# Kernel tuning notes

Hardware: AMD Instinct MI355X
Metric: run time of the kernel (lower is better)

## Reference

```python
import jax, jax.numpy as jnp
import numpy as np

RANK = 8
NUM_MORPH = 10000   # morpheme vocab (num_embeddings)
CORE_DIM = 8        # ceil(512 ** (1/3))
ORDER = 3
NUM_SURF = 50000    # word vocab (num_surfaces)
EMB_DIM = 512
LN_EPS = 1e-5
BATCH, SEQ = 8, 2048


def setup_inputs() -> dict:
    key = jax.random.key(0)
    kx, kc, kw = jax.random.split(key, 3)
    # token ids over the word vocabulary
    x = jax.random.randint(kx, (BATCH, SEQ), 0, NUM_SURF, dtype=jnp.int64)
    # word -> morpheme-id mapping, one id per tensor-train order position
    co_matrix = jax.random.randint(kc, (NUM_SURF, ORDER), 0, NUM_MORPH, dtype=jnp.int64)
    # xavier_uniform over (rank, num_morph, core_dim): fan_in = num_morph*core_dim, fan_out = rank*core_dim
    bound = float(np.sqrt(6.0 / (NUM_MORPH * CORE_DIM + RANK * CORE_DIM)))
    weight = jax.random.uniform(kw, (RANK, NUM_MORPH, CORE_DIM), dtype=jnp.float32,
                                minval=-bound, maxval=bound)
    weight = weight.at[:, 0].set(0.0)  # reset_parameters zeroes morpheme index 0
    ln_scale = jnp.ones((EMB_DIM,), dtype=jnp.float32)
    ln_bias = jnp.zeros((EMB_DIM,), dtype=jnp.float32)
    return {"x": x, "co_matrix": co_matrix, "weight": weight,
            "ln_scale": ln_scale, "ln_bias": ln_bias}


def _emb_matrix(weight, co_matrix, ln_scale, ln_bias):
    # gather all order cores at once: [rank, num_surf, order, core_dim]
    cores = weight[:, co_matrix, :]
    w = cores[:, :, 0, :]                                  # [R, S, C]
    for i in range(1, ORDER):
        # order-wise broadcast outer product, flattened feature dim grows C^i
        w = (w[:, :, :, None] * cores[:, :, i, None, :]).reshape(RANK, NUM_SURF, -1)
    w = w.sum(axis=0)[:, :EMB_DIM]                         # [S, EMB_DIM]
    mu = jnp.mean(w, axis=-1, keepdims=True)
    var = jnp.var(w, axis=-1, keepdims=True)
    return (w - mu) * jax.lax.rsqrt(var + LN_EPS) * ln_scale + ln_bias


def reference(x, co_matrix, weight, ln_scale, ln_bias):
    emb = _emb_matrix(weight, co_matrix, ln_scale, ln_bias)  # full-vocab table
    return emb[x]                                            # [B, S, EMB_DIM]
```

## Files before the change

### kernel.cpp

```cpp
#include <hip/hip_runtime.h>


#define RANK      8
#define NUM_MORPH 10000
#define EMB       512
#define LN_EPS    1e-5f
#define WPB       4
#define RSTRIDE   80000

__device__ __forceinline__ float dpp_add_b1(float v) {
    return v + __int_as_float(__builtin_amdgcn_update_dpp(
        __float_as_int(v), __float_as_int(v), 0xB1, 0xf, 0xf, false));
}
__device__ __forceinline__ float dpp_add_4e(float v) {
    return v + __int_as_float(__builtin_amdgcn_update_dpp(
        __float_as_int(v), __float_as_int(v), 0x4E, 0xf, 0xf, false));
}
__device__ __forceinline__ float dpp_add_hm(float v) {
    return v + __int_as_float(__builtin_amdgcn_update_dpp(
        __float_as_int(v), __float_as_int(v), 0x141, 0xf, 0xf, false));
}
__device__ __forceinline__ float dpp_add_m(float v) {
    return v + __int_as_float(__builtin_amdgcn_update_dpp(
        __float_as_int(v), __float_as_int(v), 0x140, 0xf, 0xf, false));
}
__device__ __forceinline__ float rdlane(float v, int l) {
    return __int_as_float(__builtin_amdgcn_readlane(__float_as_int(v), l));
}

__global__ __launch_bounds__(256) void morph_emb_kernel(
    const int* __restrict__ x,
    const int* __restrict__ co,
    const float* __restrict__ W,
    const float* __restrict__ lns,
    const float* __restrict__ lnb,
    float* __restrict__ out,
    int n_tok) {
    const int lane = threadIdx.x & 63;
    const int wid  = blockIdx.x * WPB + (threadIdx.x >> 6);
    const int tok  = (wid < n_tok) ? wid : (n_tok - 1);

    float gv[8], bv[8];
#pragma unroll
    for (int j = 0; j < 8; ++j) {
        gv[j] = lns[j * 64 + lane];
        bv[j] = lnb[j * 64 + lane];
    }

    const int s  = x[tok];
    const int m0 = co[s * 3 + 0];
    const int m1 = co[s * 3 + 1];
    const int m2 = co[s * 3 + 2];

    const float a_mine =
        W[(size_t)(lane >> 3) * RSTRIDE + (size_t)m0 * 8 + (lane & 7)];

    const float* pb = W + (size_t)m1 * 8 + (lane >> 3);
    const float* pc = W + (size_t)m2 * 8 + (lane & 7);
    float p[RANK];
#pragma unroll
    for (int r = 0; r < RANK; ++r)
        p[r] = pb[r * RSTRIDE] * pc[r * RSTRIDE];

    float acc[8] = {0.f, 0.f, 0.f, 0.f, 0.f, 0.f, 0.f, 0.f};
#pragma unroll
    for (int r = 0; r < RANK; ++r) {
#pragma unroll
        for (int j = 0; j < 8; ++j)
            acc[j] = fmaf(p[r], rdlane(a_mine, r * 8 + j), acc[j]);
    }

    float sm = 0.f, sq = 0.f;
#pragma unroll
    for (int j = 0; j < 8; ++j) { sm += acc[j]; sq += acc[j] * acc[j]; }
    sm = dpp_add_b1(sm); sq = dpp_add_b1(sq);
    sm = dpp_add_4e(sm); sq = dpp_add_4e(sq);
    sm = dpp_add_hm(sm); sq = dpp_add_hm(sq);
    sm = dpp_add_m(sm);  sq = dpp_add_m(sq);
    const float tot_s = (rdlane(sm, 0) + rdlane(sm, 16)) +
                        (rdlane(sm, 32) + rdlane(sm, 48));
    const float tot_q = (rdlane(sq, 0) + rdlane(sq, 16)) +
                        (rdlane(sq, 32) + rdlane(sq, 48));
    const float mu = tot_s * (1.0f / EMB);
    const float rs = rsqrtf(tot_q * (1.0f / EMB) - mu * mu + LN_EPS);

    if (wid < n_tok) {
        float* op = out + (size_t)wid * EMB + lane;
#pragma unroll
        for (int j = 0; j < 8; ++j)
            op[j * 64] = (acc[j] - mu) * rs * gv[j] + bv[j];
    }
}

extern "C" void kernel_launch(void* const* d_in, const int* in_sizes, int n_in,
                              void* d_out, int out_size, void* d_ws, size_t ws_size,
                              hipStream_t stream) {
    const int*   x   = (const int*)d_in[0];
    const int*   co  = (const int*)d_in[1];
    const float* W   = (const float*)d_in[2];
    const float* lns = (const float*)d_in[3];
    const float* lnb = (const float*)d_in[4];
    float*       out = (float*)d_out;

    const int n_tok  = in_sizes[0];
    const int blocks = (n_tok + WPB - 1) / WPB;
    morph_emb_kernel<<<blocks, WPB * 64, 0, stream>>>(x, co, W, lns, lnb, out, n_tok);
}
```

Baseline: 16.52 us.

## Give each lane eight contiguous outputs with vectorized loads and nontemporal stores

Measured after the change: 20.72 us. +25.4%, slower.

```diff
diff --git a/kernel.cpp b/kernel.cpp
--- a/kernel.cpp
+++ b/kernel.cpp
@@ -8,21 +8,12 @@
 #define WPB       4
 #define RSTRIDE   80000
 
-__device__ __forceinline__ float dpp_add_b1(float v) {
+typedef float f32x4 __attribute__((ext_vector_type(4)));
+
+template <int CTRL>
+__device__ __forceinline__ float dpp_add(float v) {
     return v + __int_as_float(__builtin_amdgcn_update_dpp(
-        __float_as_int(v), __float_as_int(v), 0xB1, 0xf, 0xf, false));
-}
-__device__ __forceinline__ float dpp_add_4e(float v) {
-    return v + __int_as_float(__builtin_amdgcn_update_dpp(
-        __float_as_int(v), __float_as_int(v), 0x4E, 0xf, 0xf, false));
-}
-__device__ __forceinline__ float dpp_add_hm(float v) {
-    return v + __int_as_float(__builtin_amdgcn_update_dpp(
-        __float_as_int(v), __float_as_int(v), 0x141, 0xf, 0xf, false));
-}
-__device__ __forceinline__ float dpp_add_m(float v) {
-    return v + __int_as_float(__builtin_amdgcn_update_dpp(
-        __float_as_int(v), __float_as_int(v), 0x140, 0xf, 0xf, false));
+        __float_as_int(v), __float_as_int(v), CTRL, 0xf, 0xf, false));
 }
 __device__ __forceinline__ float rdlane(float v, int l) {
     return __int_as_float(__builtin_amdgcn_readlane(__float_as_int(v), l));
@@ -40,43 +31,44 @@
     const int wid  = blockIdx.x * WPB + (threadIdx.x >> 6);
     const int tok  = (wid < n_tok) ? wid : (n_tok - 1);
 
-    float gv[8], bv[8];
-#pragma unroll
-    for (int j = 0; j < 8; ++j) {
-        gv[j] = lns[j * 64 + lane];
-        bv[j] = lnb[j * 64 + lane];
-    }
-
     const int s  = x[tok];
     const int m0 = co[s * 3 + 0];
     const int m1 = co[s * 3 + 1];
     const int m2 = co[s * 3 + 2];
 
-    const float a_mine =
-        W[(size_t)(lane >> 3) * RSTRIDE + (size_t)m0 * 8 + (lane & 7)];
+    const float* pa = W + (size_t)m0 * 8 + (lane >> 3);
+    const float* pb = W + (size_t)m1 * 8 + (lane & 7);
+    const float* pc = W + (size_t)m2 * 8;
 
-    const float* pb = W + (size_t)m1 * 8 + (lane >> 3);
-    const float* pc = W + (size_t)m2 * 8 + (lane & 7);
     float p[RANK];
+    f32x4 c0[RANK], c1[RANK];
 #pragma unroll
-    for (int r = 0; r < RANK; ++r)
-        p[r] = pb[r * RSTRIDE] * pc[r * RSTRIDE];
+    for (int r = 0; r < RANK; ++r) {
+        p[r]  = pa[r * RSTRIDE] * pb[r * RSTRIDE];
+        c0[r] = *reinterpret_cast<const f32x4*>(pc + r * RSTRIDE);
+        c1[r] = *reinterpret_cast<const f32x4*>(pc + r * RSTRIDE + 4);
+    }
 
     float acc[8] = {0.f, 0.f, 0.f, 0.f, 0.f, 0.f, 0.f, 0.f};
 #pragma unroll
     for (int r = 0; r < RANK; ++r) {
-#pragma unroll
-        for (int j = 0; j < 8; ++j)
-            acc[j] = fmaf(p[r], rdlane(a_mine, r * 8 + j), acc[j]);
+        acc[0] = fmaf(p[r], c0[r][0], acc[0]);
+        acc[1] = fmaf(p[r], c0[r][1], acc[1]);
+        acc[2] = fmaf(p[r], c0[r][2], acc[2]);
+        acc[3] = fmaf(p[r], c0[r][3], acc[3]);
+        acc[4] = fmaf(p[r], c1[r][0], acc[4]);
+        acc[5] = fmaf(p[r], c1[r][1], acc[5]);
+        acc[6] = fmaf(p[r], c1[r][2], acc[6]);
+        acc[7] = fmaf(p[r], c1[r][3], acc[7]);
     }
 
     float sm = 0.f, sq = 0.f;
 #pragma unroll
     for (int j = 0; j < 8; ++j) { sm += acc[j]; sq += acc[j] * acc[j]; }
-    sm = dpp_add_b1(sm); sq = dpp_add_b1(sq);
-    sm = dpp_add_4e(sm); sq = dpp_add_4e(sq);
-    sm = dpp_add_hm(sm); sq = dpp_add_hm(sq);
-    sm = dpp_add_m(sm);  sq = dpp_add_m(sq);
+    sm = dpp_add<0xB1>(sm);  sq = dpp_add<0xB1>(sq);
+    sm = dpp_add<0x4E>(sm);  sq = dpp_add<0x4E>(sq);
+    sm = dpp_add<0x141>(sm); sq = dpp_add<0x141>(sq);
+    sm = dpp_add<0x140>(sm); sq = dpp_add<0x140>(sq);
     const float tot_s = (rdlane(sm, 0) + rdlane(sm, 16)) +
                         (rdlane(sm, 32) + rdlane(sm, 48));
     const float tot_q = (rdlane(sq, 0) + rdlane(sq, 16)) +
@@ -84,11 +76,25 @@
     const float mu = tot_s * (1.0f / EMB);
     const float rs = rsqrtf(tot_q * (1.0f / EMB) - mu * mu + LN_EPS);
 
+    const int e = lane << 3;
+    const f32x4 g0 = *reinterpret_cast<const f32x4*>(lns + e);
+    const f32x4 g1 = *reinterpret_cast<const f32x4*>(lns + e + 4);
+    const f32x4 b0 = *reinterpret_cast<const f32x4*>(lnb + e);
+    const f32x4 b1 = *reinterpret_cast<const f32x4*>(lnb + e + 4);
+
     if (wid < n_tok) {
-        float* op = out + (size_t)wid * EMB + lane;
-#pragma unroll
-        for (int j = 0; j < 8; ++j)
-            op[j * 64] = (acc[j] - mu) * rs * gv[j] + bv[j];
+        f32x4 o0, o1;
+        o0[0] = (acc[0] - mu) * rs * g0[0] + b0[0];
+        o0[1] = (acc[1] - mu) * rs * g0[1] + b0[1];
+        o0[2] = (acc[2] - mu) * rs * g0[2] + b0[2];
+        o0[3] = (acc[3] - mu) * rs * g0[3] + b0[3];
+        o1[0] = (acc[4] - mu) * rs * g1[0] + b1[0];
+        o1[1] = (acc[5] - mu) * rs * g1[1] + b1[1];
+        o1[2] = (acc[6] - mu) * rs * g1[2] + b1[2];
+        o1[3] = (acc[7] - mu) * rs * g1[3] + b1[3];
+        f32x4* op = reinterpret_cast<f32x4*>(out + (size_t)wid * EMB + e);
+        __builtin_nontemporal_store(o0, op);
+        __builtin_nontemporal_store(o1, op + 1);
     }
 }
 
```
